# Kernel tuning notes

Measured on AMD Instinct MI355X. Metric: run time of the kernel, lower is better.

## Reference

```python
import jax, jax.numpy as jnp
import numpy as np

HEADS = 4
DIM_HEAD = 32
SCALE = DIM_HEAD ** -0.5


def setup_inputs() -> dict:
    key = jax.random.key(0)
    ks = jax.random.split(key, 7)
    b, c, h, w = 2, 256, 64, 64
    time_dim = 512
    hidden = HEADS * DIM_HEAD  # 128
    return {
        "x": jax.random.normal(ks[0], (b, c, h, w), jnp.float32),
        "time_emb": jax.random.normal(ks[1], (b, time_dim), jnp.float32),
        "w_mlp": jax.random.normal(ks[2], (2 * c, time_dim), jnp.float32) * 0.02,
        "b_mlp": jax.random.normal(ks[3], (2 * c,), jnp.float32) * 0.02,
        "w_qkv": jax.random.normal(ks[4], (3 * hidden, c), jnp.float32) * 0.05,
        "w_out": jax.random.normal(ks[5], (c, hidden), jnp.float32) * 0.05,
        "b_out": jax.random.normal(ks[6], (c,), jnp.float32) * 0.02,
    }


def reference(x, time_emb, w_mlp, b_mlp, w_qkv, w_out, b_out):
    b, c, h, w = x.shape
    n = h * w
    # FiLM conditioning: SiLU -> Linear -> chunk into (scale, shift)
    t = jax.nn.silu(time_emb) @ w_mlp.T + b_mlp            # [b, 2c]
    scale, shift = jnp.split(t, 2, axis=1)                  # [b, c] each
    x = x * (scale + 1.0)[:, :, None, None] + shift[:, :, None, None]
    # 1x1 conv QKV projection (no bias)
    qkv = jnp.einsum('oc,bchw->bohw', w_qkv, x)             # [b, 3*hidden, h, w]
    q, k, v = jnp.split(qkv, 3, axis=1)                     # [b, hidden, h, w]
    def to_heads(t):
        return t.reshape(b, HEADS, DIM_HEAD, n)             # b h d (x y)
    q, k, v = to_heads(q) * SCALE, to_heads(k), to_heads(v)
    sim = jnp.einsum('bhdi,bhdj->bhij', q, k)               # [b, h, n, n]
    attn = jax.nn.softmax(sim, axis=-1)
    out = jnp.einsum('bhij,bhdj->bhid', attn, v)            # [b, h, n, d]
    # b h (x y) d -> b (h d) x y
    out = out.transpose(0, 1, 3, 2).reshape(b, HEADS * DIM_HEAD, h, w)
    return jnp.einsum('oc,bchw->bohw', w_out, out) + b_out[None, :, None, None]
```

## Files before the change

kernel.cpp:

```cpp
#include <hip/hip_runtime.h>


typedef __bf16 bf16x8 __attribute__((ext_vector_type(8)));
typedef float  f32x16 __attribute__((ext_vector_type(16)));
typedef unsigned uint2v __attribute__((ext_vector_type(2)));

#define MFMA(a, b, c) __builtin_amdgcn_mfma_f32_32x32x16_bf16((a), (b), (c), 0, 0, 0)
#define PLSWAP(a, b) __builtin_amdgcn_permlane32_swap((a), (b), false, false)

static constexpr float kLOG2E = 1.4426950408889634f;
static constexpr float kSCALE = 0.17677669529663687f;

__device__ __forceinline__ unsigned short bf16r(float x) {
  union { float f; unsigned u; } v; v.f = x;
  return (unsigned short)((v.u + 0x7FFFu + ((v.u >> 16) & 1u)) >> 16);
}
__device__ __forceinline__ float fast_silu(float x) {
  return x / (1.0f + __builtin_amdgcn_exp2f(-x * kLOG2E));
}
__device__ __forceinline__ f32x16 zero16() {
  f32x16 z;
#pragma unroll
  for (int i = 0; i < 16; ++i) z[i] = 0.0f;
  return z;
}
__device__ __forceinline__ bf16x8 ld_frag(const unsigned short* p) {
  return *reinterpret_cast<const bf16x8*>(p);
}

__global__ __launch_bounds__(256) void prep(const float* __restrict__ x,
                                            unsigned short* __restrict__ xT,
                                            const float* __restrict__ te,
                                            const float* __restrict__ w_mlp,
                                            const float* __restrict__ b_mlp,
                                            float* __restrict__ fparams) {
  __shared__ unsigned short lds[64][66];
  int bid = blockIdx.x;
  if (bid < 32) {
    int g = bid * 256 + threadIdx.x;
    int pair = g >> 3, ks = g & 7;
    int b = pair >> 9, o = pair & 511;
    const float4* w4 = (const float4*)(w_mlp + (size_t)o * 512 + ks * 64);
    const float4* t4 = (const float4*)(te + (size_t)b * 512 + ks * 64);
    float s = 0.0f;
#pragma unroll 4
    for (int k = 0; k < 16; ++k) {
      float4 wv = w4[k];
      float4 tv = t4[k];
      s += wv.x * fast_silu(tv.x) + wv.y * fast_silu(tv.y) +
           wv.z * fast_silu(tv.z) + wv.w * fast_silu(tv.w);
    }
    s += __shfl_xor(s, 1, 64);
    s += __shfl_xor(s, 2, 64);
    s += __shfl_xor(s, 4, 64);
    if (ks == 0) {
      float t_val = s + b_mlp[o];
      fparams[b * 512 + o] = (o < 256) ? (t_val + 1.0f) : t_val;
    }
    return;
  }
  int bid2 = bid - 32;
  int p0 = (bid2 & 63) * 64;
  int c0 = ((bid2 >> 6) & 3) * 64;
  int b  = bid2 >> 8;
  int t = threadIdx.x;
  int pl = t & 63, cw = t >> 6;
  const float* xb = x + ((size_t)b * 256 + c0) * 4096 + p0;
#pragma unroll
  for (int r = 0; r < 16; ++r) {
    int cl = cw + r * 4;
    lds[pl][cl] = bf16r(xb[(size_t)cl * 4096 + pl]);
  }
  __syncthreads();
  unsigned short* out = xT + ((size_t)b * 4096 + p0) * 256 + c0;
#pragma unroll
  for (int rep = 0; rep < 2; ++rep) {
    int ch = t + rep * 256;
    int pr = ch >> 3, cc = (ch & 7) * 8;
    union { unsigned short u[8]; uint4 v; } pk;
#pragma unroll
    for (int i = 0; i < 8; ++i) pk.u[i] = lds[pr][cc + i];
    *(uint4*)(out + (size_t)pr * 256 + cc) = pk.v;
  }
}

__global__ __launch_bounds__(256) void film2(const float* __restrict__ w_qkv,
                                             const float* __restrict__ fparams,
                                             const float* __restrict__ w_out,
                                             unsigned short* __restrict__ Aeff,
                                             float* __restrict__ qb,
                                             unsigned short* __restrict__ WoBf) {
  int tid = blockIdx.x * 256 + threadIdx.x;
  if (tid < 3072) {
    int row = tid >> 2, cs = tid & 3;
    int b = row / 384, o = row % 384;
    float qs = (o < 128) ? (kSCALE * kLOG2E) : 1.0f;
    const float4* wr  = (const float4*)(w_qkv + (size_t)o * 256);
    const float4* sc4 = (const float4*)(fparams + b * 512);
    const float4* sh4 = (const float4*)(fparams + b * 512 + 256);
    unsigned short* arow = Aeff + ((size_t)b * 384 + o) * 256;
    float acc = 0.0f;
#pragma unroll 4
    for (int i = 0; i < 16; ++i) {
      int c4 = cs * 16 + i;
      float4 wv = wr[c4], scv = sc4[c4], shv = sh4[c4];
      acc += wv.x * shv.x + wv.y * shv.y + wv.z * shv.z + wv.w * shv.w;
      union { unsigned short u[4]; unsigned long long q; } pk;
      pk.u[0] = bf16r(wv.x * scv.x * qs);
      pk.u[1] = bf16r(wv.y * scv.y * qs);
      pk.u[2] = bf16r(wv.z * scv.z * qs);
      pk.u[3] = bf16r(wv.w * scv.w * qs);
      *(unsigned long long*)(arow + c4 * 4) = pk.q;
    }
    acc += __shfl_xor(acc, 1, 64);
    acc += __shfl_xor(acc, 2, 64);
    if (cs == 0) qb[b * 384 + o] = acc * qs;
  } else {
    int t = tid - 3072;
    const float4* src = (const float4*)(w_out + (size_t)t * 64);
    unsigned short* dst = WoBf + (size_t)t * 64;
#pragma unroll 4
    for (int i = 0; i < 16; ++i) {
      float4 v = src[i];
      union { unsigned short u[4]; unsigned long long q; } pk;
      pk.u[0] = bf16r(v.x); pk.u[1] = bf16r(v.y);
      pk.u[2] = bf16r(v.z); pk.u[3] = bf16r(v.w);
      *(unsigned long long*)(dst + i * 4) = pk.q;
    }
  }
}

__global__ __launch_bounds__(64) void qkv_gemm(const unsigned short* __restrict__ Aeff,
                                               const float* __restrict__ qb,
                                               const unsigned short* __restrict__ xT,
                                               unsigned short* __restrict__ Qb,
                                               unsigned short* __restrict__ Kb,
                                               unsigned short* __restrict__ Vt) {
  int bid = blockIdx.x;
  int o_blk = bid % 12;
  int rest = bid / 12;
  int b = rest & 1, p_blk = rest >> 1;
  int l = threadIdx.x, col = l & 31, hi = l >> 5;

  const unsigned short* Ab = Aeff + ((size_t)b * 384 + o_blk * 32) * 256;
  const unsigned short* Bb = xT + ((size_t)b * 4096 + p_blk * 32) * 256;

  f32x16 acc = zero16();
#pragma unroll
  for (int kc = 0; kc < 256; kc += 16) {
    bf16x8 a0 = ld_frag(Ab + (size_t)col * 256 + kc + hi * 8);
    bf16x8 b0 = ld_frag(Bb + (size_t)col * 256 + kc + hi * 8);
    acc = MFMA(a0, b0, acc);
  }

  int obase = o_blk * 32;
  int sec = obase >> 7;
  int head = (obase & 127) >> 5;
  size_t bh = (size_t)b * 4 + head;
  int p = p_blk * 32 + col;
  if (sec < 2) {
    unsigned short* dst = (sec == 0 ? Qb : Kb) + (bh * 4096 + p) * 32;
#pragma unroll
    for (int g = 0; g < 4; ++g) {
      int dbase = 8 * g + 4 * hi;
      union { unsigned short u[4]; unsigned long long q; } pk;
#pragma unroll
      for (int r = 0; r < 4; ++r)
        pk.u[r] = bf16r(acc[4 * g + r] + qb[b * 384 + obase + dbase + r]);
      *(unsigned long long*)(dst + dbase) = pk.q;
    }
  } else {
    unsigned short* dst = Vt + bh * 32 * 4096;
#pragma unroll
    for (int reg = 0; reg < 16; ++reg) {
      int d = (reg & 3) + 8 * (reg >> 2) + 4 * hi;
      dst[(size_t)d * 4096 + p] = bf16r(acc[reg] + qb[b * 384 + obase + d]);
    }
  }
}

__global__ __launch_bounds__(256, 4) void attn(const unsigned short* __restrict__ Qb,
                                               const unsigned short* __restrict__ Kb,
                                               const unsigned short* __restrict__ Vt,
                                               unsigned short* __restrict__ Ob) {
  __shared__ float Olds[4][16][64];
  __shared__ float llds[4][64];

  int bid = blockIdx.x;
  int bh = bid >> 7;
  int q0 = (bid & 127) * 32;
  int w = threadIdx.x >> 6;
  int l = threadIdx.x & 63, col = l & 31, hi = l >> 5;

  const unsigned short* Qp = Qb + ((size_t)bh * 4096 + q0) * 32;
  bf16x8 qf0 = ld_frag(Qp + col * 32 + hi * 8);
  bf16x8 qf1 = ld_frag(Qp + col * 32 + 16 + hi * 8);

  const unsigned short* kp =
      Kb + (size_t)bh * 131072 + ((size_t)(w * 1024 + col)) * 32 + hi * 8;
  const unsigned short* vp =
      Vt + (size_t)bh * 131072 + (size_t)col * 4096 + w * 1024 + hi * 8;

  const f32x16 zc = zero16();
  f32x16 O = zero16();
  float lsum = 0.0f;

  bf16x8 ka0 = ld_frag(kp);
  bf16x8 ka1 = ld_frag(kp + 16);
  bf16x8 va0 = ld_frag(vp);
  bf16x8 va1 = ld_frag(vp + 16);

  for (int it = 0; it < 32; ++it) {
    f32x16 S = MFMA(ka0, qf0, zc);
    S = MFMA(ka1, qf1, S);

    kp += 1024; vp += 32;
    bf16x8 nka0 = ld_frag(kp);
    bf16x8 nka1 = ld_frag(kp + 16);
    bf16x8 nva0 = ld_frag(vp);
    bf16x8 nva1 = ld_frag(vp + 16);

#pragma unroll
    for (int i = 0; i < 16; ++i) S[i] = __builtin_amdgcn_exp2f(S[i]);
    float s0 = (S[0] + S[1]) + (S[2] + S[3]);
    float s1 = (S[4] + S[5]) + (S[6] + S[7]);
    float s2 = (S[8] + S[9]) + (S[10] + S[11]);
    float s3 = (S[12] + S[13]) + (S[14] + S[15]);
    lsum += (s0 + s1) + (s2 + s3);

    union { __bf16 h[16]; unsigned u[8]; } pu;
#pragma unroll
    for (int i = 0; i < 16; ++i) pu.h[i] = (__bf16)S[i];
    uint2v r0 = PLSWAP(pu.u[0], pu.u[2]);
    uint2v r1 = PLSWAP(pu.u[1], pu.u[3]);
    uint2v r2 = PLSWAP(pu.u[4], pu.u[6]);
    uint2v r3 = PLSWAP(pu.u[5], pu.u[7]);
    union { unsigned u[4]; bf16x8 v; } B0, B1;
    B0.u[0] = r0[0]; B0.u[1] = r1[0]; B0.u[2] = r0[1]; B0.u[3] = r1[1];
    B1.u[0] = r2[0]; B1.u[1] = r3[0]; B1.u[2] = r2[1]; B1.u[3] = r3[1];

    O = MFMA(va0, B0.v, O);
    O = MFMA(va1, B1.v, O);

    ka0 = nka0; ka1 = nka1; va0 = nva0; va1 = nva1;
  }

  uint2v lr = PLSWAP(__float_as_uint(lsum), __float_as_uint(lsum));
  float lt = __uint_as_float(lr[0]) + __uint_as_float(lr[1]);

#pragma unroll
  for (int i = 0; i < 16; ++i) Olds[w][i][l] = O[i];
  llds[w][l] = lt;
  __syncthreads();

  float L = llds[0][l] + llds[1][l] + llds[2][l] + llds[3][l];
  float inv = 1.0f / L;

  union { unsigned short u[4]; unsigned long long q; } pk4;
#pragma unroll
  for (int r = 0; r < 4; ++r) {
    int reg = 4 * w + r;
    float v = Olds[0][reg][l] + Olds[1][reg][l] + Olds[2][reg][l] + Olds[3][reg][l];
    pk4.u[r] = bf16r(v * inv);
  }
  unsigned short* dst = Ob + ((size_t)bh * 4096 + q0 + col) * 32 + 8 * w + 4 * hi;
  *(unsigned long long*)dst = pk4.q;
}

__global__ __launch_bounds__(64) void out_gemm(const unsigned short* __restrict__ Wo,
                                               const unsigned short* __restrict__ Ob,
                                               const float* __restrict__ b_out,
                                               float* __restrict__ out) {
  int bid = blockIdx.x;
  int o_blk = bid & 7;
  int rest = bid >> 3;
  int b = rest & 1, p_blk = rest >> 1;
  int l = threadIdx.x, col = l & 31, hi = l >> 5;

  const unsigned short* Ab = Wo + (size_t)(o_blk * 32) * 128;
  f32x16 acc = zero16();
#pragma unroll
  for (int kc = 0; kc < 128; kc += 16) {
    int head = kc >> 5;
    int doff = (kc & 16) + hi * 8;
    const unsigned short* Bb =
        Ob + (((size_t)b * 4 + head) * 4096 + p_blk * 32) * 32 + doff;
    bf16x8 a0 = ld_frag(Ab + (size_t)col * 128 + kc + hi * 8);
    bf16x8 b0 = ld_frag(Bb + (size_t)col * 32);
    acc = MFMA(a0, b0, acc);
  }
  int p = p_blk * 32 + col;
#pragma unroll
  for (int reg = 0; reg < 16; ++reg) {
    int o = o_blk * 32 + (reg & 3) + 8 * (reg >> 2) + 4 * hi;
    out[((size_t)b * 256 + o) * 4096 + p] = acc[reg] + b_out[o];
  }
}

extern "C" void kernel_launch(void* const* d_in, const int* in_sizes, int n_in,
                              void* d_out, int out_size, void* d_ws, size_t ws_size,
                              hipStream_t stream) {
  const float* x     = (const float*)d_in[0];
  const float* te    = (const float*)d_in[1];
  const float* w_mlp = (const float*)d_in[2];
  const float* b_mlp = (const float*)d_in[3];
  const float* w_qkv = (const float*)d_in[4];
  const float* w_out = (const float*)d_in[5];
  const float* b_out = (const float*)d_in[6];

  char* ws = (char*)d_ws;
  float*          fparams = (float*)(ws + 0);
  float*          qb      = (float*)(ws + 4096);
  unsigned short* Aeff    = (unsigned short*)(ws + 8192);
  unsigned short* WoBf    = (unsigned short*)(ws + 401408);
  unsigned short* xT      = (unsigned short*)(ws + 466944);
  unsigned short* Qb      = (unsigned short*)(ws + 4661248);
  unsigned short* Kb      = (unsigned short*)(ws + 6758400);
  unsigned short* Vt      = (unsigned short*)(ws + 8855552);
  unsigned short* Ob      = (unsigned short*)(ws + 10952704);
  float* out = (float*)d_out;

  hipLaunchKernelGGL(prep, dim3(544), dim3(256), 0, stream, x, xT, te, w_mlp,
                     b_mlp, fparams);
  hipLaunchKernelGGL(film2, dim3(14), dim3(256), 0, stream, w_qkv, fparams, w_out,
                     Aeff, qb, WoBf);
  hipLaunchKernelGGL(qkv_gemm, dim3(3072), dim3(64), 0, stream, Aeff, qb, xT, Qb, Kb, Vt);
  hipLaunchKernelGGL(attn, dim3(1024), dim3(256), 0, stream, Qb, Kb, Vt, Ob);
  hipLaunchKernelGGL(out_gemm, dim3(2048), dim3(64), 0, stream, WoBf, Ob, b_out, out);
}
```

Measured before the change: 151.7 us.

## Split attention keys across eight waves and widen FiLM weight prep

The attention kernel now runs 8 waves per block instead of 4. Each wave handles 512 keys, and the loop is unrolled by two with separate K/V prefetch registers, so two score/PV chains interleave. The final cross-wave reduction is spread over 8 waves, each writing two output values. The film2 prep kernel uses 32 lanes per output row instead of 4, with a wider shuffle reduction, to fix its very low parallelism. The risk is a larger shared-memory reduction and more register pressure per block.

Result: no change. 150.3 us (-1.0%).

```diff
diff --git a/kernel.cpp b/kernel.cpp
--- a/kernel.cpp
+++ b/kernel.cpp
@@ -91,8 +91,8 @@
                                              float* __restrict__ qb,
                                              unsigned short* __restrict__ WoBf) {
   int tid = blockIdx.x * 256 + threadIdx.x;
-  if (tid < 3072) {
-    int row = tid >> 2, cs = tid & 3;
+  if (tid < 24576) {
+    int row = tid >> 5, cs = tid & 31;
     int b = row / 384, o = row % 384;
     float qs = (o < 128) ? (kSCALE * kLOG2E) : 1.0f;
     const float4* wr  = (const float4*)(w_qkv + (size_t)o * 256);
@@ -100,9 +100,9 @@
     const float4* sh4 = (const float4*)(fparams + b * 512 + 256);
     unsigned short* arow = Aeff + ((size_t)b * 384 + o) * 256;
     float acc = 0.0f;
-#pragma unroll 4
-    for (int i = 0; i < 16; ++i) {
-      int c4 = cs * 16 + i;
+#pragma unroll
+    for (int j = 0; j < 2; ++j) {
+      int c4 = cs * 2 + j;
       float4 wv = wr[c4], scv = sc4[c4], shv = sh4[c4];
       acc += wv.x * shv.x + wv.y * shv.y + wv.z * shv.z + wv.w * shv.w;
       union { unsigned short u[4]; unsigned long long q; } pk;
@@ -114,9 +114,12 @@
     }
     acc += __shfl_xor(acc, 1, 64);
     acc += __shfl_xor(acc, 2, 64);
+    acc += __shfl_xor(acc, 4, 64);
+    acc += __shfl_xor(acc, 8, 64);
+    acc += __shfl_xor(acc, 16, 64);
     if (cs == 0) qb[b * 384 + o] = acc * qs;
   } else {
-    int t = tid - 3072;
+    int t = tid - 24576;
     const float4* src = (const float4*)(w_out + (size_t)t * 64);
     unsigned short* dst = WoBf + (size_t)t * 64;
 #pragma unroll 4
@@ -179,12 +182,35 @@
   }
 }
 
-__global__ __launch_bounds__(256, 4) void attn(const unsigned short* __restrict__ Qb,
-                                               const unsigned short* __restrict__ Kb,
-                                               const unsigned short* __restrict__ Vt,
-                                               unsigned short* __restrict__ Ob) {
-  __shared__ float Olds[4][16][64];
-  __shared__ float llds[4][64];
+__device__ __forceinline__ void softmax_pv(f32x16 S, bf16x8 va0, bf16x8 va1,
+                                           f32x16& O, float& lsum) {
+#pragma unroll
+  for (int i = 0; i < 16; ++i) S[i] = __builtin_amdgcn_exp2f(S[i]);
+  float s0 = (S[0] + S[1]) + (S[2] + S[3]);
+  float s1 = (S[4] + S[5]) + (S[6] + S[7]);
+  float s2 = (S[8] + S[9]) + (S[10] + S[11]);
+  float s3 = (S[12] + S[13]) + (S[14] + S[15]);
+  lsum += (s0 + s1) + (s2 + s3);
+  union { __bf16 h[16]; unsigned u[8]; } pu;
+#pragma unroll
+  for (int i = 0; i < 16; ++i) pu.h[i] = (__bf16)S[i];
+  uint2v r0 = PLSWAP(pu.u[0], pu.u[2]);
+  uint2v r1 = PLSWAP(pu.u[1], pu.u[3]);
+  uint2v r2 = PLSWAP(pu.u[4], pu.u[6]);
+  uint2v r3 = PLSWAP(pu.u[5], pu.u[7]);
+  union { unsigned u[4]; bf16x8 v; } B0, B1;
+  B0.u[0] = r0[0]; B0.u[1] = r1[0]; B0.u[2] = r0[1]; B0.u[3] = r1[1];
+  B1.u[0] = r2[0]; B1.u[1] = r3[0]; B1.u[2] = r2[1]; B1.u[3] = r3[1];
+  O = MFMA(va0, B0.v, O);
+  O = MFMA(va1, B1.v, O);
+}
+
+__global__ __launch_bounds__(512) void attn(const unsigned short* __restrict__ Qb,
+                                            const unsigned short* __restrict__ Kb,
+                                            const unsigned short* __restrict__ Vt,
+                                            unsigned short* __restrict__ Ob) {
+  __shared__ float Olds[8][16][64];
+  __shared__ float llds[8][64];
 
   int bid = blockIdx.x;
   int bh = bid >> 7;
@@ -197,52 +223,37 @@
   bf16x8 qf1 = ld_frag(Qp + col * 32 + 16 + hi * 8);
 
   const unsigned short* kp =
-      Kb + (size_t)bh * 131072 + ((size_t)(w * 1024 + col)) * 32 + hi * 8;
+      Kb + (size_t)bh * 131072 + (size_t)(w * 512 + col) * 32 + hi * 8;
   const unsigned short* vp =
-      Vt + (size_t)bh * 131072 + (size_t)col * 4096 + w * 1024 + hi * 8;
+      Vt + (size_t)bh * 131072 + (size_t)col * 4096 + w * 512 + hi * 8;
 
   const f32x16 zc = zero16();
   f32x16 O = zero16();
   float lsum = 0.0f;
 
-  bf16x8 ka0 = ld_frag(kp);
-  bf16x8 ka1 = ld_frag(kp + 16);
-  bf16x8 va0 = ld_frag(vp);
-  bf16x8 va1 = ld_frag(vp + 16);
-
-  for (int it = 0; it < 32; ++it) {
+  bf16x8 ka0 = ld_frag(kp),      ka1 = ld_frag(kp + 16);
+  bf16x8 va0 = ld_frag(vp),      va1 = ld_frag(vp + 16);
+  kp += 1024; vp += 32;
+  bf16x8 kb0 = ld_frag(kp),      kb1 = ld_frag(kp + 16);
+  bf16x8 vb0 = ld_frag(vp),      vb1 = ld_frag(vp + 16);
+
+  for (int it = 0; it < 8; ++it) {
     f32x16 S = MFMA(ka0, qf0, zc);
     S = MFMA(ka1, qf1, S);
-
     kp += 1024; vp += 32;
-    bf16x8 nka0 = ld_frag(kp);
-    bf16x8 nka1 = ld_frag(kp + 16);
-    bf16x8 nva0 = ld_frag(vp);
-    bf16x8 nva1 = ld_frag(vp + 16);
-
-#pragma unroll
-    for (int i = 0; i < 16; ++i) S[i] = __builtin_amdgcn_exp2f(S[i]);
-    float s0 = (S[0] + S[1]) + (S[2] + S[3]);
-    float s1 = (S[4] + S[5]) + (S[6] + S[7]);
-    float s2 = (S[8] + S[9]) + (S[10] + S[11]);
-    float s3 = (S[12] + S[13]) + (S[14] + S[15]);
-    lsum += (s0 + s1) + (s2 + s3);
-
-    union { __bf16 h[16]; unsigned u[8]; } pu;
-#pragma unroll
-    for (int i = 0; i < 16; ++i) pu.h[i] = (__bf16)S[i];
-    uint2v r0 = PLSWAP(pu.u[0], pu.u[2]);
-    uint2v r1 = PLSWAP(pu.u[1], pu.u[3]);
-    uint2v r2 = PLSWAP(pu.u[4], pu.u[6]);
-    uint2v r3 = PLSWAP(pu.u[5], pu.u[7]);
-    union { unsigned u[4]; bf16x8 v; } B0, B1;
-    B0.u[0] = r0[0]; B0.u[1] = r1[0]; B0.u[2] = r0[1]; B0.u[3] = r1[1];
-    B1.u[0] = r2[0]; B1.u[1] = r3[0]; B1.u[2] = r2[1]; B1.u[3] = r3[1];
-
-    O = MFMA(va0, B0.v, O);
-    O = MFMA(va1, B1.v, O);
-
-    ka0 = nka0; ka1 = nka1; va0 = nva0; va1 = nva1;
+    ka0 = ld_frag(kp); ka1 = ld_frag(kp + 16);
+    va0_next:;
+    bf16x8 pva0 = va0, pva1 = va1;
+    va0 = ld_frag(vp); va1 = ld_frag(vp + 16);
+    softmax_pv(S, pva0, pva1, O, lsum);
+
+    f32x16 S2 = MFMA(kb0, qf0, zc);
+    S2 = MFMA(kb1, qf1, S2);
+    kp += 1024; vp += 32;
+    kb0 = ld_frag(kp); kb1 = ld_frag(kp + 16);
+    bf16x8 pvb0 = vb0, pvb1 = vb1;
+    vb0 = ld_frag(vp); vb1 = ld_frag(vp + 16);
+    softmax_pv(S2, pvb0, pvb1, O, lsum);
   }
 
   uint2v lr = PLSWAP(__float_as_uint(lsum), __float_as_uint(lsum));
@@ -253,18 +264,23 @@
   llds[w][l] = lt;
   __syncthreads();
 
-  float L = llds[0][l] + llds[1][l] + llds[2][l] + llds[3][l];
+  float L = ((llds[0][l] + llds[1][l]) + (llds[2][l] + llds[3][l])) +
+            ((llds[4][l] + llds[5][l]) + (llds[6][l] + llds[7][l]));
   float inv = 1.0f / L;
 
-  union { unsigned short u[4]; unsigned long long q; } pk4;
-#pragma unroll
-  for (int r = 0; r < 4; ++r) {
-    int reg = 4 * w + r;
-    float v = Olds[0][reg][l] + Olds[1][reg][l] + Olds[2][reg][l] + Olds[3][reg][l];
-    pk4.u[r] = bf16r(v * inv);
-  }
-  unsigned short* dst = Ob + ((size_t)bh * 4096 + q0 + col) * 32 + 8 * w + 4 * hi;
-  *(unsigned long long*)dst = pk4.q;
+  int reg0 = 2 * w;
+  float v0 = 0.0f, v1 = 0.0f;
+#pragma unroll
+  for (int i = 0; i < 8; ++i) {
+    v0 += Olds[i][reg0][l];
+    v1 += Olds[i][reg0 + 1][l];
+  }
+  int based = 8 * (w >> 1) + 2 * (w & 1) + 4 * hi;
+  unsigned short* dst = Ob + ((size_t)bh * 4096 + q0 + col) * 32 + based;
+  union { unsigned short u[2]; unsigned q; } pk2;
+  pk2.u[0] = bf16r(v0 * inv);
+  pk2.u[1] = bf16r(v1 * inv);
+  *(unsigned*)dst = pk2.q;
 }
 
 __global__ __launch_bounds__(64) void out_gemm(const unsigned short* __restrict__ Wo,
@@ -322,9 +338,9 @@
 
   hipLaunchKernelGGL(prep, dim3(544), dim3(256), 0, stream, x, xT, te, w_mlp,
                      b_mlp, fparams);
-  hipLaunchKernelGGL(film2, dim3(14), dim3(256), 0, stream, w_qkv, fparams, w_out,
+  hipLaunchKernelGGL(film2, dim3(98), dim3(256), 0, stream, w_qkv, fparams, w_out,
                      Aeff, qb, WoBf);
   hipLaunchKernelGGL(qkv_gemm, dim3(3072), dim3(64), 0, stream, Aeff, qb, xT, Qb, Kb, Vt);
-  hipLaunchKernelGGL(attn, dim3(1024), dim3(256), 0, stream, Qb, Kb, Vt, Ob);
+  hipLaunchKernelGGL(attn, dim3(1024), dim3(512), 0, stream, Qb, Kb, Vt, Ob);
   hipLaunchKernelGGL(out_gemm, dim3(2048), dim3(64), 0, stream, WoBf, Ob, b_out, out);
 }
```
